# Performance work log

Hardware: AMD Instinct MI355X
Metric: run time of the kernel (lower is better)

Reference implementation:

```python
import jax, jax.numpy as jnp
import numpy as np

DIM = 256
HEADS = 8
WIN = 8
HIDDEN = 1024
EPS = 1e-5

def _rel_pos_index(w):
    coords = np.stack(np.meshgrid(np.arange(w), np.arange(w), indexing='ij'))  # [2,w,w]
    cf = coords.reshape(2, -1)
    rel = cf[:, :, None] - cf[:, None, :]  # [2,N,N]
    rel = rel.transpose(1, 2, 0)
    rel[:, :, 0] += w - 1
    rel[:, :, 1] += w - 1
    rel[:, :, 0] *= 2 * w - 1
    return jnp.asarray(rel.sum(-1))  # [N,N] int

REL_IDX = _rel_pos_index(WIN)

def _layernorm(x, g, b):
    mu = jnp.mean(x, -1, keepdims=True)
    var = jnp.mean(jnp.square(x - mu), -1, keepdims=True)
    return (x - mu) * jax.lax.rsqrt(var + EPS) * g + b

def setup_inputs() -> dict:
    key = jax.random.key(0)
    ks = jax.random.split(key, 12)
    s = 0.02
    return {
        'x': jax.random.normal(ks[0], (16, 4096, 256), jnp.float32),
        'H': 64,
        'W': 64,
        'ln1_g': jnp.ones((DIM,), jnp.float32),
        'ln1_b': jnp.zeros((DIM,), jnp.float32),
        'qkv_w': jax.random.normal(ks[1], (DIM, 3 * DIM), jnp.float32) * s,
        'proj_w': jax.random.normal(ks[2], (DIM, DIM), jnp.float32) * s,
        'proj_b': jnp.zeros((DIM,), jnp.float32),
        'rel_bias_table': jax.random.normal(ks[3], ((2 * WIN - 1) ** 2, HEADS), jnp.float32) * s,
        'ln2_g': jnp.ones((DIM,), jnp.float32),
        'ln2_b': jnp.zeros((DIM,), jnp.float32),
        'fc1_w': jax.random.normal(ks[4], (DIM, HIDDEN), jnp.float32) * s,
        'fc1_b': jnp.zeros((HIDDEN,), jnp.float32),
        'fc2_w': jax.random.normal(ks[5], (HIDDEN, DIM), jnp.float32) * s,
        'fc2_b': jnp.zeros((DIM,), jnp.float32),
    }

def reference(x, H, W, ln1_g, ln1_b, qkv_w, proj_w, proj_b, rel_bias_table,
              ln2_g, ln2_b, fc1_w, fc1_b, fc2_w, fc2_b):
    B, L, C = x.shape
    w = WIN
    N = w * w
    head_dim = C // HEADS
    scale = head_dim ** -0.5

    shortcut = x
    h = _layernorm(x, ln1_g, ln1_b).reshape(B, H, W, C)
    # H, W chosen divisible by window_size -> pad_h = pad_w = 0 (faithful fast path)
    # window partition: [B*nW, N, C]
    h = h.reshape(B, H // w, w, W // w, w, C).transpose(0, 1, 3, 2, 4, 5)
    xw = h.reshape(-1, N, C)
    Bw = xw.shape[0]

    qkv = (xw @ qkv_w).reshape(Bw, N, 3, HEADS, head_dim)
    q = qkv[:, :, 0].transpose(0, 2, 1, 3) * scale  # [Bw,h,N,d]
    k = qkv[:, :, 1].transpose(0, 2, 1, 3)
    v = qkv[:, :, 2].transpose(0, 2, 1, 3)

    attn = jnp.einsum('bhnd,bhmd->bhnm', q, k)
    bias = rel_bias_table[REL_IDX.reshape(-1)].reshape(N, N, HEADS).transpose(2, 0, 1)
    attn = jax.nn.softmax(attn + bias[None], axis=-1)
    out = jnp.einsum('bhnm,bhmd->bhnd', attn, v).transpose(0, 2, 1, 3).reshape(Bw, N, C)
    out = out @ proj_w + proj_b

    # window reverse
    out = out.reshape(B, H // w, W // w, w, w, C).transpose(0, 1, 3, 2, 4, 5)
    out = out.reshape(B, L, C)

    x = shortcut + out
    h2 = _layernorm(x, ln2_g, ln2_b)
    mlp = jax.nn.gelu(h2 @ fc1_w + fc1_b, approximate=False) @ fc2_w + fc2_b
    return x + mlp
```

## Files before the change

### kernel.cpp

```cpp
#include <hip/hip_runtime.h>
#include <hip/hip_bf16.h>

typedef __attribute__((ext_vector_type(8))) short bf16x8;
typedef __attribute__((ext_vector_type(4))) float f32x4;

typedef __attribute__((address_space(3))) void LdsVoid;
typedef const __attribute__((address_space(1))) void GblVoid;

__device__ __forceinline__ void gload16(const void* g, void* l) {
  __builtin_amdgcn_global_load_lds((GblVoid*)g, (LdsVoid*)l, 16, 0, 0);
}

__device__ __forceinline__ unsigned short f2bf(float f) {
  union { float f; unsigned int u; } x; x.f = f;
  unsigned int r = (x.u + 0x7fffu + ((x.u >> 16) & 1u)) >> 16;
  return (unsigned short)r;
}

__device__ __forceinline__ float gelu_f(float t) {
  float u = t * (0.7978845608028654f + 0.03567740814f * t * t);
  float e = __expf(2.0f * u);
  float th = 1.0f - 2.0f / (e + 1.0f);
  return 0.5f * t * (1.0f + th);
}

__global__ __launch_bounds__(256) void prep_w(
    const float* __restrict__ qw, const float* __restrict__ pw,
    const float* __restrict__ f1, const float* __restrict__ f2,
    unsigned short* __restrict__ out) {
  int idx = blockIdx.x * 256 + threadIdx.x;
  if (idx < 196608) { int n = idx >> 8, k = idx & 255; out[idx] = f2bf(qw[k * 768 + n]); return; }
  int i2 = idx - 196608;
  if (i2 < 65536) { int n = i2 >> 8, k = i2 & 255; out[idx] = f2bf(pw[k * 256 + n]); return; }
  int i3 = i2 - 65536;
  if (i3 < 262144) { int n = i3 >> 8, k = i3 & 255; out[idx] = f2bf(f1[k * 1024 + n]); return; }
  int i4 = i3 - 262144;
  { int n = i4 >> 10, k = i4 & 1023; out[idx] = f2bf(f2[k * 256 + n]); }
}

__global__ __launch_bounds__(256) void ln1_kernel(
    const float* __restrict__ x, const float* __restrict__ g, const float* __restrict__ b,
    unsigned short* __restrict__ xn) {
  int lane = threadIdx.x & 63, wid = threadIdx.x >> 6;
  size_t t = (size_t)blockIdx.x * 4 + wid;
  float4 v = ((const float4*)(x + t * 256))[lane];
  float s = v.x + v.y + v.z + v.w;
  #pragma unroll
  for (int m = 1; m < 64; m <<= 1) s += __shfl_xor(s, m);
  float mean = s * (1.0f / 256.0f);
  float dx = v.x - mean, dy = v.y - mean, dz = v.z - mean, dw = v.w - mean;
  float q = dx * dx + dy * dy + dz * dz + dw * dw;
  #pragma unroll
  for (int m = 1; m < 64; m <<= 1) q += __shfl_xor(q, m);
  float rstd = rsqrtf(q * (1.0f / 256.0f) + 1e-5f);
  float4 gg = ((const float4*)g)[lane];
  float4 bb = ((const float4*)b)[lane];
  unsigned int o0 = f2bf(dx * rstd * gg.x + bb.x) | ((unsigned int)f2bf(dy * rstd * gg.y + bb.y) << 16);
  unsigned int o1 = f2bf(dz * rstd * gg.z + bb.z) | ((unsigned int)f2bf(dw * rstd * gg.w + bb.w) << 16);
  int bI = (int)(t >> 12), rem = (int)t & 4095, y = rem >> 6, xc = rem & 63;
  size_t r = ((size_t)(bI * 64 + (y >> 3) * 8 + (xc >> 3))) * 64 + (y & 7) * 8 + (xc & 7);
  uint2 o; o.x = o0; o.y = o1;
  ((uint2*)(xn + r * 256))[lane] = o;
}

template <int EPI>
__global__ __launch_bounds__(256) void gemm_bt(
    const unsigned short* __restrict__ A, const unsigned short* __restrict__ Bt,
    unsigned short* __restrict__ outb, float* __restrict__ outf,
    const float* __restrict__ bias, const float* __restrict__ xres,
    int M, int N, int K) {
  __shared__ __align__(16) unsigned short lds[2 * 16384];
  const int tid = threadIdx.x;
  const int lane = tid & 63, wid = tid >> 6;
  const int cl = lane & 15, cg = lane >> 4;
  const unsigned nwg = gridDim.x * gridDim.y;
  const unsigned orig = blockIdx.y * gridDim.x + blockIdx.x;
  const unsigned virt = (orig & 7) * (nwg >> 3) + (orig >> 3);
  const unsigned bx = virt % gridDim.x, by = virt / gridDim.x;
  const size_t m0 = (size_t)by * 128;
  const size_t n0 = (size_t)bx * 128;
  const int wr = wid >> 1, wc = wid & 1;
  f32x4 acc[4][4] = {};

  const int r8 = lane >> 3;
  const int gsw = ((lane & 7) ^ r8) * 8;
  const unsigned short* aStage = A + (m0 + wid * 32 + r8) * K + gsw;
  const unsigned short* bStage = Bt + (n0 + wid * 32 + r8) * K + gsw;
  const size_t jstep = (size_t)8 * K;
  const int nt = K >> 6;

  #define STAGE(T, B)                                                   \
    { const int ko_ = (T) * 64;                                         \
      unsigned short* la_ = lds + (B) * 16384 + wid * 2048;             \
      unsigned short* lb_ = la_ + 8192;                                 \
      _Pragma("unroll")                                                 \
      for (int j = 0; j < 4; ++j) {                                     \
        gload16(aStage + ko_ + j * jstep, la_ + j * 512);               \
        gload16(bStage + ko_ + j * jstep, lb_ + j * 512);               \
      } }

  bf16x8 af[2][4], bfr[2][4];
  #define READF(B)                                                          \
    { const unsigned short* base_ = lds + (B) * 16384;                      \
      _Pragma("unroll")                                                     \
      for (int kk = 0; kk < 2; ++kk)                                        \
        _Pragma("unroll")                                                   \
        for (int i = 0; i < 4; ++i) {                                       \
          const int sl_ = ((kk * 4 + cg) ^ (cl & 7)) * 8;                   \
          af[kk][i]  = *(const bf16x8*)(base_ + (wr * 64 + i * 16 + cl) * 64 + sl_);        \
          bfr[kk][i] = *(const bf16x8*)(base_ + 8192 + (wc * 64 + i * 16 + cl) * 64 + sl_); \
        } }

  #define MFMAS()                                                           \
    { _Pragma("unroll")                                                     \
      for (int kk = 0; kk < 2; ++kk)                                        \
        _Pragma("unroll")                                                   \
        for (int mi = 0; mi < 4; ++mi)                                      \
          _Pragma("unroll")                                                 \
          for (int ni = 0; ni < 4; ++ni)                                    \
            acc[mi][ni] = __builtin_amdgcn_mfma_f32_16x16x32_bf16(bfr[kk][ni], af[kk][mi], acc[mi][ni], 0, 0, 0); }

  STAGE(0, 0);
  STAGE(1, 1);
  for (int t = 0; t < nt; ++t) {
    if (t == nt - 1) { asm volatile("s_waitcnt vmcnt(0)" ::: "memory"); }
    else             { asm volatile("s_waitcnt vmcnt(8)" ::: "memory"); }
    __builtin_amdgcn_s_barrier();
    READF(t & 1);
    __builtin_amdgcn_sched_barrier(0);
    asm volatile("s_waitcnt lgkmcnt(0)" ::: "memory");
    __builtin_amdgcn_s_barrier();
    __builtin_amdgcn_sched_barrier(0);
    if (t + 2 < nt) STAGE(t + 2, t & 1);
    MFMAS();
  }
  #undef STAGE
  #undef READF
  #undef MFMAS

  #pragma unroll
  for (int mi = 0; mi < 4; ++mi) {
    const size_t row = m0 + wr * 64 + mi * 16 + cl;
    #pragma unroll
    for (int ni = 0; ni < 4; ++ni) {
      const size_t col = n0 + wc * 64 + ni * 16 + cg * 4;
      f32x4 v = acc[mi][ni];
      if (EPI == 0) {
        uint2 o;
        o.x = f2bf(v[0]) | ((unsigned int)f2bf(v[1]) << 16);
        o.y = f2bf(v[2]) | ((unsigned int)f2bf(v[3]) << 16);
        *(uint2*)&outb[row * N + col] = o;
      } else if (EPI == 1) {
        float4 bb = *(const float4*)&bias[col];
        float g0 = gelu_f(v[0] + bb.x), g1 = gelu_f(v[1] + bb.y);
        float g2 = gelu_f(v[2] + bb.z), g3 = gelu_f(v[3] + bb.w);
        uint2 o;
        o.x = f2bf(g0) | ((unsigned int)f2bf(g1) << 16);
        o.y = f2bf(g2) | ((unsigned int)f2bf(g3) << 16);
        *(uint2*)&outb[row * N + col] = o;
      } else if (EPI == 3) {
        float4 bb = *(const float4*)&bias[col];
        float4* p = (float4*)&outf[row * N + col];
        float4 old = *p;
        old.x += v[0] + bb.x; old.y += v[1] + bb.y;
        old.z += v[2] + bb.z; old.w += v[3] + bb.w;
        *p = old;
      } else if (EPI == 4) {
        int winr = (int)(row >> 6), pos = (int)(row & 63);
        int bI = winr >> 6, wy = (winr >> 3) & 7, wx = winr & 7;
        size_t tt = (size_t)bI * 4096 + (size_t)(wy * 8 + (pos >> 3)) * 64 + wx * 8 + (pos & 7);
        float4 bb = *(const float4*)&bias[col];
        float4 xr = *(const float4*)&xres[tt * 256 + col];
        float4 o;
        o.x = v[0] + bb.x + xr.x; o.y = v[1] + bb.y + xr.y;
        o.z = v[2] + bb.z + xr.z; o.w = v[3] + bb.w + xr.w;
        *(float4*)&outf[tt * 256 + col] = o;
      }
    }
  }
}

__global__ __launch_bounds__(256) void attn_win(
    const unsigned short* __restrict__ qkv, const float* __restrict__ table,
    unsigned short* __restrict__ out) {
  __shared__ float tbl[1800];
  __shared__ __align__(16) unsigned short p_lds[4][64 * 72];
  __shared__ __align__(16) unsigned short vt_lds[4][32 * 72];
  const int tid = threadIdx.x, lane = tid & 63, wid = tid >> 6;
  const int cl = lane & 15, cg = lane >> 4;
  for (int i = tid; i < 1800; i += 256) tbl[i] = table[i];
  __syncthreads();
  const size_t wbase = (size_t)blockIdx.x * 64;
  unsigned short* P = p_lds[wid];
  unsigned short* VT = vt_lds[wid];
  const float scale = 0.17677669529663687f;

  for (int hh = 0; hh < 2; ++hh) {
    const int h = wid + hh * 4;
    const int qoff = h * 32, koff = 256 + h * 32, voff = 512 + h * 32;
    bf16x8 qf[4], kf[4];
    #pragma unroll
    for (int mi = 0; mi < 4; ++mi)
      qf[mi] = *(const bf16x8*)&qkv[(wbase + mi * 16 + cl) * 768 + qoff + cg * 8];
    #pragma unroll
    for (int nj = 0; nj < 4; ++nj)
      kf[nj] = *(const bf16x8*)&qkv[(wbase + nj * 16 + cl) * 768 + koff + cg * 8];
    f32x4 S[4][4] = {};
    #pragma unroll
    for (int mi = 0; mi < 4; ++mi)
      #pragma unroll
      for (int nj = 0; nj < 4; ++nj)
        S[mi][nj] = __builtin_amdgcn_mfma_f32_16x16x32_bf16(qf[mi], kf[nj], S[mi][nj], 0, 0, 0);

    {
      const unsigned short* vrow = &qkv[(wbase + lane) * 768 + voff];
      unsigned short tmp[32];
      #pragma unroll
      for (int p = 0; p < 4; ++p) *(uint4*)&tmp[p * 8] = ((const uint4*)vrow)[p];
      #pragma unroll
      for (int d = 0; d < 32; ++d) VT[d * 72 + lane] = tmp[d];
    }

    #pragma unroll
    for (int mi = 0; mi < 4; ++mi) {
      #pragma unroll
      for (int r = 0; r < 4; ++r) {
        const int i = mi * 16 + cg * 4 + r;
        const int yi = i >> 3, xi = i & 7;
        float v[4];
        float m = -1e30f;
        #pragma unroll
        for (int nj = 0; nj < 4; ++nj) {
          const int j = nj * 16 + cl;
          const int yj = j >> 3, xj = j & 7;
          float bia = tbl[((yi - yj + 7) * 15 + (xi - xj + 7)) * 8 + h];
          v[nj] = S[mi][nj][r] * scale + bia;
          m = fmaxf(m, v[nj]);
        }
        #pragma unroll
        for (int mk = 1; mk < 16; mk <<= 1) m = fmaxf(m, __shfl_xor(m, mk));
        float s = 0.0f;
        #pragma unroll
        for (int nj = 0; nj < 4; ++nj) { v[nj] = expf(v[nj] - m); s += v[nj]; }
        #pragma unroll
        for (int mk = 1; mk < 16; mk <<= 1) s += __shfl_xor(s, mk);
        const float rinv = 1.0f / s;
        #pragma unroll
        for (int nj = 0; nj < 4; ++nj) P[i * 72 + nj * 16 + cl] = f2bf(v[nj] * rinv);
      }
    }

    f32x4 O[4][2] = {};
    #pragma unroll
    for (int ks = 0; ks < 2; ++ks) {
      bf16x8 pa[4], vb[2];
      #pragma unroll
      for (int mi = 0; mi < 4; ++mi)
        pa[mi] = *(const bf16x8*)&P[(mi * 16 + cl) * 72 + ks * 32 + cg * 8];
      #pragma unroll
      for (int nd = 0; nd < 2; ++nd)
        vb[nd] = *(const bf16x8*)&VT[(nd * 16 + cl) * 72 + ks * 32 + cg * 8];
      #pragma unroll
      for (int mi = 0; mi < 4; ++mi)
        #pragma unroll
        for (int nd = 0; nd < 2; ++nd)
          O[mi][nd] = __builtin_amdgcn_mfma_f32_16x16x32_bf16(vb[nd], pa[mi], O[mi][nd], 0, 0, 0);
    }

    #pragma unroll
    for (int mi = 0; mi < 4; ++mi)
      #pragma unroll
      for (int nd = 0; nd < 2; ++nd) {
        uint2 o;
        o.x = f2bf(O[mi][nd][0]) | ((unsigned int)f2bf(O[mi][nd][1]) << 16);
        o.y = f2bf(O[mi][nd][2]) | ((unsigned int)f2bf(O[mi][nd][3]) << 16);
        *(uint2*)&out[(wbase + mi * 16 + cl) * 256 + h * 32 + nd * 16 + cg * 4] = o;
      }
  }
}

__global__ __launch_bounds__(256) void ln2_kernel(
    const float* __restrict__ x2, const float* __restrict__ g, const float* __restrict__ b,
    unsigned short* __restrict__ h2) {
  int lane = threadIdx.x & 63, wid = threadIdx.x >> 6;
  size_t t = (size_t)blockIdx.x * 4 + wid;
  float4 v = ((const float4*)(x2 + t * 256))[lane];
  float s = v.x + v.y + v.z + v.w;
  #pragma unroll
  for (int m = 1; m < 64; m <<= 1) s += __shfl_xor(s, m);
  float mean = s * (1.0f / 256.0f);
  float dx = v.x - mean, dy = v.y - mean, dz = v.z - mean, dw = v.w - mean;
  float q = dx * dx + dy * dy + dz * dz + dw * dw;
  #pragma unroll
  for (int m = 1; m < 64; m <<= 1) q += __shfl_xor(q, m);
  float rstd = rsqrtf(q * (1.0f / 256.0f) + 1e-5f);
  float4 gg = ((const float4*)g)[lane];
  float4 bb = ((const float4*)b)[lane];
  uint2 o;
  o.x = f2bf(dx * rstd * gg.x + bb.x) | ((unsigned int)f2bf(dy * rstd * gg.y + bb.y) << 16);
  o.y = f2bf(dz * rstd * gg.z + bb.z) | ((unsigned int)f2bf(dw * rstd * gg.w + bb.w) << 16);
  ((uint2*)(h2 + t * 256))[lane] = o;
}

extern "C" void kernel_launch(void* const* d_in, const int* in_sizes, int n_in,
                              void* d_out, int out_size, void* d_ws, size_t ws_size,
                              hipStream_t stream) {
  (void)in_sizes; (void)n_in; (void)out_size; (void)ws_size;
  const float* x       = (const float*)d_in[0];
  const float* ln1_g   = (const float*)d_in[3];
  const float* ln1_b   = (const float*)d_in[4];
  const float* qkv_w   = (const float*)d_in[5];
  const float* proj_w  = (const float*)d_in[6];
  const float* proj_b  = (const float*)d_in[7];
  const float* rel_tbl = (const float*)d_in[8];
  const float* ln2_g   = (const float*)d_in[9];
  const float* ln2_b   = (const float*)d_in[10];
  const float* fc1_w   = (const float*)d_in[11];
  const float* fc1_b   = (const float*)d_in[12];
  const float* fc2_w   = (const float*)d_in[13];
  const float* fc2_b   = (const float*)d_in[14];
  float* out = (float*)d_out;

  char* ws = (char*)d_ws;
  const size_t OFF_XN   = 1572864;
  const size_t OFF_QKV  = OFF_XN + 33554432;
  const size_t OFF_ATTN = OFF_QKV + 100663296;
  unsigned short* Wt      = (unsigned short*)ws;
  unsigned short* xn      = (unsigned short*)(ws + OFF_XN);
  unsigned short* h2      = xn;
  unsigned short* qkv     = (unsigned short*)(ws + OFF_QKV);
  unsigned short* fc1out  = (unsigned short*)(ws + OFF_QKV);
  unsigned short* attnout = (unsigned short*)(ws + OFF_ATTN);

  prep_w<<<3072, 256, 0, stream>>>(qkv_w, proj_w, fc1_w, fc2_w, Wt);
  ln1_kernel<<<16384, 256, 0, stream>>>(x, ln1_g, ln1_b, xn);
  gemm_bt<0><<<dim3(6, 512), 256, 0, stream>>>(xn, Wt, qkv, nullptr, nullptr, nullptr, 65536, 768, 256);
  attn_win<<<1024, 256, 0, stream>>>(qkv, rel_tbl, attnout);
  gemm_bt<4><<<dim3(2, 512), 256, 0, stream>>>(attnout, Wt + 196608, nullptr, out, proj_b, x, 65536, 256, 256);
  ln2_kernel<<<16384, 256, 0, stream>>>(out, ln2_g, ln2_b, h2);
  gemm_bt<1><<<dim3(8, 512), 256, 0, stream>>>(h2, Wt + 262144, fc1out, nullptr, fc1_b, nullptr, 65536, 1024, 256);
  gemm_bt<3><<<dim3(2, 512), 256, 0, stream>>>(fc1out, Wt + 524288, nullptr, out, fc2_b, nullptr, 65536, 256, 1024);
}
```

Before: 449.4 us.

## Halve GEMM K-tile to 32 and use fast exp/rcp intrinsics

The bf16 GEMM K-step per stage drops from 64 to 32. This halves LDS usage (64KB to 32KB) and the fragment registers, and the swizzle and wait counts are rewritten to match the 4-lane row layout. The likely aim is more resident workgroups per CU, paid for with twice as many barrier/wait iterations and fewer MFMAs per sync. Separately, softmax and GELU switch to __expf and hardware reciprocal, which are cheaper but slightly less precise.

```diff
diff --git a/kernel.cpp b/kernel.cpp
--- a/kernel.cpp
+++ b/kernel.cpp
@@ -20,7 +20,7 @@
 __device__ __forceinline__ float gelu_f(float t) {
   float u = t * (0.7978845608028654f + 0.03567740814f * t * t);
   float e = __expf(2.0f * u);
-  float th = 1.0f - 2.0f / (e + 1.0f);
+  float th = 1.0f - 2.0f * __builtin_amdgcn_rcpf(e + 1.0f);
   return 0.5f * t * (1.0f + th);
 }
 
@@ -69,7 +69,7 @@
     unsigned short* __restrict__ outb, float* __restrict__ outf,
     const float* __restrict__ bias, const float* __restrict__ xres,
     int M, int N, int K) {
-  __shared__ __align__(16) unsigned short lds[2 * 16384];
+  __shared__ __align__(16) unsigned short lds[2 * 8192];
   const int tid = threadIdx.x;
   const int lane = tid & 63, wid = tid >> 6;
   const int cl = lane & 15, cg = lane >> 4;
@@ -82,49 +82,44 @@
   const int wr = wid >> 1, wc = wid & 1;
   f32x4 acc[4][4] = {};
 
-  const int r8 = lane >> 3;
-  const int gsw = ((lane & 7) ^ r8) * 8;
-  const unsigned short* aStage = A + (m0 + wid * 32 + r8) * K + gsw;
-  const unsigned short* bStage = Bt + (n0 + wid * 32 + r8) * K + gsw;
-  const size_t jstep = (size_t)8 * K;
-  const int nt = K >> 6;
+  const int r4 = lane >> 2;
+  const int gsw = ((lane & 3) ^ ((r4 >> 1) & 3)) * 8;
+  const unsigned short* aStage = A + (m0 + wid * 32 + r4) * K + gsw;
+  const unsigned short* bStage = Bt + (n0 + wid * 32 + r4) * K + gsw;
+  const size_t jstep = (size_t)16 * K;
+  const int nt = K >> 5;
 
   #define STAGE(T, B)                                                   \
-    { const int ko_ = (T) * 64;                                         \
-      unsigned short* la_ = lds + (B) * 16384 + wid * 2048;             \
-      unsigned short* lb_ = la_ + 8192;                                 \
-      _Pragma("unroll")                                                 \
-      for (int j = 0; j < 4; ++j) {                                     \
-        gload16(aStage + ko_ + j * jstep, la_ + j * 512);               \
-        gload16(bStage + ko_ + j * jstep, lb_ + j * 512);               \
+    { const int ko_ = (T) * 32;                                         \
+      unsigned short* la_ = lds + (B) * 8192 + wid * 1024;              \
+      unsigned short* lb_ = la_ + 4096;                                 \
+      gload16(aStage + ko_, la_);                                       \
+      gload16(aStage + ko_ + jstep, la_ + 512);                         \
+      gload16(bStage + ko_, lb_);                                       \
+      gload16(bStage + ko_ + jstep, lb_ + 512); }
+
+  bf16x8 af[4], bfr[4];
+  const int sl_ = (cg ^ ((cl >> 1) & 3)) * 8;
+  #define READF(B)                                                          \
+    { const unsigned short* base_ = lds + (B) * 8192;                       \
+      _Pragma("unroll")                                                     \
+      for (int i = 0; i < 4; ++i) {                                         \
+        af[i]  = *(const bf16x8*)(base_ + (wr * 64 + i * 16 + cl) * 32 + sl_);        \
+        bfr[i] = *(const bf16x8*)(base_ + 4096 + (wc * 64 + i * 16 + cl) * 32 + sl_); \
       } }
-
-  bf16x8 af[2][4], bfr[2][4];
-  #define READF(B)                                                          \
-    { const unsigned short* base_ = lds + (B) * 16384;                      \
-      _Pragma("unroll")                                                     \
-      for (int kk = 0; kk < 2; ++kk)                                        \
-        _Pragma("unroll")                                                   \
-        for (int i = 0; i < 4; ++i) {                                       \
-          const int sl_ = ((kk * 4 + cg) ^ (cl & 7)) * 8;                   \
-          af[kk][i]  = *(const bf16x8*)(base_ + (wr * 64 + i * 16 + cl) * 64 + sl_);        \
-          bfr[kk][i] = *(const bf16x8*)(base_ + 8192 + (wc * 64 + i * 16 + cl) * 64 + sl_); \
-        } }
 
   #define MFMAS()                                                           \
     { _Pragma("unroll")                                                     \
-      for (int kk = 0; kk < 2; ++kk)                                        \
+      for (int mi = 0; mi < 4; ++mi)                                        \
         _Pragma("unroll")                                                   \
-        for (int mi = 0; mi < 4; ++mi)                                      \
-          _Pragma("unroll")                                                 \
-          for (int ni = 0; ni < 4; ++ni)                                    \
-            acc[mi][ni] = __builtin_amdgcn_mfma_f32_16x16x32_bf16(bfr[kk][ni], af[kk][mi], acc[mi][ni], 0, 0, 0); }
+        for (int ni = 0; ni < 4; ++ni)                                      \
+          acc[mi][ni] = __builtin_amdgcn_mfma_f32_16x16x32_bf16(bfr[ni], af[mi], acc[mi][ni], 0, 0, 0); }
 
   STAGE(0, 0);
   STAGE(1, 1);
   for (int t = 0; t < nt; ++t) {
     if (t == nt - 1) { asm volatile("s_waitcnt vmcnt(0)" ::: "memory"); }
-    else             { asm volatile("s_waitcnt vmcnt(8)" ::: "memory"); }
+    else             { asm volatile("s_waitcnt vmcnt(4)" ::: "memory"); }
     __builtin_amdgcn_s_barrier();
     READF(t & 1);
     __builtin_amdgcn_sched_barrier(0);
@@ -241,10 +236,10 @@
         for (int mk = 1; mk < 16; mk <<= 1) m = fmaxf(m, __shfl_xor(m, mk));
         float s = 0.0f;
         #pragma unroll
-        for (int nj = 0; nj < 4; ++nj) { v[nj] = expf(v[nj] - m); s += v[nj]; }
+        for (int nj = 0; nj < 4; ++nj) { v[nj] = __expf(v[nj] - m); s += v[nj]; }
         #pragma unroll
         for (int mk = 1; mk < 16; mk <<= 1) s += __shfl_xor(s, mk);
-        const float rinv = 1.0f / s;
+        const float rinv = __builtin_amdgcn_rcpf(s);
         #pragma unroll
         for (int nj = 0; nj < 4; ++nj) P[i * 72 + nj * 16 + cl] = f2bf(v[nj] * rinv);
       }
```

After: 430.6 us. 1.04x faster.
